# Performance work log

Measured on AMD Instinct MI355X. Metric: run time of the kernel, lower is better.

Reference implementation:

```python
import jax, jax.numpy as jnp
import numpy as np

H = 16   # num_heads
D = 16   # key_dim == output_dim (required by the module's reshape)
F = 64   # input feature dim


def setup_inputs() -> dict:
    key = jax.random.key(0)
    ks = jax.random.split(key, 8)
    B, N, Kn = 4, 4096, 32
    scale = 1.0 / np.sqrt(F)
    return {
        "inp": jax.random.normal(ks[0], (B, N, Kn, F), dtype=jnp.float32),
        "query": jax.random.normal(ks[1], (B, N, F), dtype=jnp.float32),
        "Wq": jax.random.normal(ks[2], (F, H * D), dtype=jnp.float32) * scale,
        "bq": jnp.zeros((H * D,), dtype=jnp.float32),
        "Wk": jax.random.normal(ks[3], (F, H * D), dtype=jnp.float32) * scale,
        "bk": jnp.zeros((H * D,), dtype=jnp.float32),
        "Wv": jax.random.normal(ks[4], (F, H * D), dtype=jnp.float32) * scale,
        "bv": jnp.zeros((H * D,), dtype=jnp.float32),
    }


def reference(inp, query, Wq, bq, Wk, bk, Wv, bv):
    B, N, Kn, _ = inp.shape
    # Dense projections
    Q = query @ Wq + bq                    # [B, N, H*D]
    K = inp @ Wk + bk                      # [B, N, Kn, H*D]
    V = inp @ Wv + bv                      # [B, N, Kn, H*D]
    # Faithful reshape (plain reshape of last dims, as in the TF code)
    Q = Q.reshape(B, N, H, 1, D)           # query broadcast axis of size 1
    K = K.reshape(B, N, H, Kn, D)
    V = V.reshape(B, N, H, Kn, D)
    # scaled dot-product attention per point over its Kn neighbors
    w = jnp.einsum('bnhqd,bnhkd->bnhqk', Q, K) / jnp.sqrt(jnp.float32(D))
    w = jax.nn.softmax(w, axis=-1)         # [B, N, H, 1, Kn]
    out = jnp.einsum('bnhqk,bnhkd->bnhqd', w, V)  # [B, N, H, 1, D]
    return out.reshape(B, N, H * D)
```

## Files before the change

kernel.cpp:

```cpp
#include <hip/hip_runtime.h>

#define KN 32
#define FF 64
#define CC 256
#define KV_STRIDE 260
#define VOFF (KN * KV_STRIDE)
#define NITER 16
#define QSTRIDE 264
#define WSTRIDE 36


typedef __attribute__((ext_vector_type(8)))  short bf16x8;
typedef __attribute__((ext_vector_type(16))) float f32x16;
typedef __attribute__((ext_vector_type(4)))  float f32x4;

__device__ inline unsigned short f2bf(float f) {
    union { float f; unsigned u; } v; v.f = f;
    unsigned u = v.u + 0x7fffu + ((v.u >> 16) & 1u);
    return (unsigned short)(u >> 16);
}
__device__ inline unsigned cvt_pk_bf16(float a, float b) {
    unsigned r;
    asm("v_cvt_pk_bf16_f32 %0, %1, %2" : "=v"(r) : "v"(a), "v"(b));
    return r;
}
__device__ inline bf16x8 pack8(float4 a, float4 b) {
    union { bf16x8 v; unsigned u[4]; } r;
    r.u[0] = cvt_pk_bf16(a.x, a.y);  r.u[1] = cvt_pk_bf16(a.z, a.w);
    r.u[2] = cvt_pk_bf16(b.x, b.y);  r.u[3] = cvt_pk_bf16(b.z, b.w);
    return r.v;
}

__device__ inline void lds_barrier() {
    asm volatile("s_waitcnt lgkmcnt(0)" ::: "memory");
    __builtin_amdgcn_s_barrier();
}

__global__ __launch_bounds__(256, 2)
void attn_one(const float* __restrict__ inp,
              const float* __restrict__ query,
              const float* __restrict__ Wq,
              const float* __restrict__ bq,
              const float* __restrict__ Wk,
              const float* __restrict__ bk,
              const float* __restrict__ Wv,
              const float* __restrict__ bv,
              float* __restrict__ out, int nPoints)
{
    __shared__ float kvS[2 * KN * KV_STRIDE];
    __shared__ unsigned short qAllS[NITER * QSTRIDE];
    __shared__ float wS[16 * WSTRIDE];

    const int tid  = threadIdx.x;
    const int wave = tid >> 6;
    const int L    = tid & 63;
    const int Lm   = L & 31;
    const int Lh   = L >> 5;
    const int h    = tid >> 4;
    const int d    = tid & 15;
    const int bid  = blockIdx.x;
    const int grid = gridDim.x;

    float* qIn = kvS;
    {
        const int i  = tid >> 4;
        const int f4 = (tid & 15) * 4;
        const int p  = bid + i * grid;
        if (p < nPoints)
            *(float4*)(qIn + i * 68 + f4) =
                *(const float4*)(query + (size_t)p * FF + f4);
    }

    float4 pf[8];
    {
        const float* arow = inp + (size_t)bid * (KN * FF) + Lm * FF + Lh * 8;
#pragma unroll
        for (int s = 0; s < 4; ++s) {
            pf[2 * s]     = *(const float4*)(arow + s * 16);
            pf[2 * s + 1] = *(const float4*)(arow + s * 16 + 4);
        }
    }

    bf16x8 Bf[4][4];
    float  bias[4];
#pragma unroll
    for (int t = 0; t < 4; ++t) {
        const float* W  = (t < 2) ? Wk : Wv;
        const float* bb = (t < 2) ? bk : bv;
        const int ch    = (2 * wave + (t & 1)) * 32 + Lm;
        bias[t] = bb[ch];
#pragma unroll
        for (int s = 0; s < 4; ++s) {
            union { bf16x8 v; unsigned u[4]; } r;
#pragma unroll
            for (int jj = 0; jj < 4; ++jj) {
                const int f = s * 16 + Lh * 8 + 2 * jj;
                r.u[jj] = cvt_pk_bf16(W[(size_t)f * CC + ch], W[(size_t)(f + 1) * CC + ch]);
            }
            Bf[t][s] = r.v;
        }
    }

    const int nq = L & 15;
    const int kq = (L >> 4) * 8;
    bf16x8 Bq[4][2];
    float  bqv[4];
#pragma unroll
    for (int tt = 0; tt < 4; ++tt) {
        const int ch = wave * 64 + tt * 16 + nq;
        bqv[tt] = bq[ch];
#pragma unroll
        for (int s = 0; s < 2; ++s) {
            union { bf16x8 v; unsigned u[4]; } r;
#pragma unroll
            for (int jj = 0; jj < 4; ++jj) {
                const int f = s * 32 + kq + 2 * jj;
                r.u[jj] = cvt_pk_bf16(Wq[(size_t)f * CC + ch], Wq[(size_t)(f + 1) * CC + ch]);
            }
            Bq[tt][s] = r.v;
        }
    }

    __syncthreads();

    {
        bf16x8 Aq[2];
        const int im = L & 15;
#pragma unroll
        for (int s = 0; s < 2; ++s) {
            const float* qr = qIn + im * 68 + s * 32 + kq;
            Aq[s] = pack8(*(const float4*)qr, *(const float4*)(qr + 4));
        }
#pragma unroll
        for (int tt = 0; tt < 4; ++tt) {
            f32x4 qa = {bqv[tt], bqv[tt], bqv[tt], bqv[tt]};
#pragma unroll
            for (int s = 0; s < 2; ++s)
                qa = __builtin_amdgcn_mfma_f32_16x16x32_bf16(Aq[s], Bq[tt][s], qa, 0, 0, 0);
            const int ch = wave * 64 + tt * 16 + nq;
#pragma unroll
            for (int r = 0; r < 4; ++r) {
                const int ip = (L >> 4) * 4 + r;
                qAllS[ip * QSTRIDE + ch] = f2bf(qa[r] * 0.25f);
            }
        }
    }
    __syncthreads();

    const int sR = d & 7;
    const int j0 = 2 * h + (d >> 3);

    for (int it = 0, p = bid; p < nPoints; ++it, p += grid) {
        bf16x8 Af[4];
#pragma unroll
        for (int s = 0; s < 4; ++s) Af[s] = pack8(pf[2 * s], pf[2 * s + 1]);

        const int pn = p + grid;
        if (pn < nPoints) {
            const float* arow = inp + (size_t)pn * (KN * FF) + Lm * FF + Lh * 8;
#pragma unroll
            for (int s = 0; s < 4; ++s) {
                pf[2 * s]     = *(const float4*)(arow + s * 16);
                pf[2 * s + 1] = *(const float4*)(arow + s * 16 + 4);
            }
        }

        f32x16 acc[4];
#pragma unroll
        for (int t = 0; t < 4; ++t)
#pragma unroll
            for (int r = 0; r < 16; ++r) acc[t][r] = bias[t];
#pragma unroll
        for (int s = 0; s < 4; ++s)
#pragma unroll
            for (int t = 0; t < 4; ++t)
                acc[t] = __builtin_amdgcn_mfma_f32_32x32x16_bf16(Af[s], Bf[t][s], acc[t], 0, 0, 0);

#pragma unroll
        for (int t = 0; t < 4; ++t) {
            const int s8 = 2 * wave + (t & 1);
            const int col = (t < 2)
                ? s8 * 32 + (((Lm >> 2) ^ s8) << 2) + (Lm & 3)
                : s8 * 32 + Lm;
            float* dstbase = kvS + ((t < 2) ? 0 : VOFF);
#pragma unroll
            for (int r = 0; r < 16; ++r) {
                const int jrow = (r & 3) + 8 * (r >> 2) + 4 * Lh;
                dstbase[jrow * KV_STRIDE + col] = acc[t][r];
            }
        }

        const unsigned short* qp = qAllS + it * QSTRIDE + h * 16;
        uint4 qA = *(const uint4*)qp;
        uint4 qB = *(const uint4*)(qp + 8);

        lds_barrier();

        const float* kb = kvS + j0 * KV_STRIDE + sR * 32;
        float4 ck[8];
#pragma unroll
        for (int w = 0; w < 8; ++w)
            ck[w] = *(const float4*)(kb + (((w ^ sR)) << 2));

        union { uint4 v; unsigned u[4]; } ua, ub;
        ua.v = qA;  ub.v = qB;
        float qv[16];
#pragma unroll
        for (int j = 0; j < 4; ++j) {
            qv[2 * j]     = __uint_as_float(ua.u[j] << 16);
            qv[2 * j + 1] = __uint_as_float(ua.u[j] & 0xffff0000u);
            qv[8 + 2 * j]     = __uint_as_float(ub.u[j] << 16);
            qv[8 + 2 * j + 1] = __uint_as_float(ub.u[j] & 0xffff0000u);
        }

        float l0a = 0.f, l0b = 0.f, l1a = 0.f, l1b = 0.f;
#pragma unroll
        for (int i = 0; i < 16; i += 2) {
            l0a = fmaf(qv[i],     ck[i >> 2][i & 3],             l0a);
            l0b = fmaf(qv[i + 1], ck[(i + 1) >> 2][(i + 1) & 3], l0b);
            l1a = fmaf(qv[i],     ck[4 + (i >> 2)][i & 3],             l1a);
            l1b = fmaf(qv[i + 1], ck[4 + ((i + 1) >> 2)][(i + 1) & 3], l1b);
        }
        const float l0 = l0a + l0b;
        const float l1 = l1a + l1b;

        float m = fmaxf(l0, l1);
        m = fmaxf(m, __shfl_xor(m, 1));
        m = fmaxf(m, __shfl_xor(m, 2));
        m = fmaxf(m, __shfl_xor(m, 4));
        m = fmaxf(m, __shfl_xor(m, 8));
        float e0 = __expf(l0 - m), e1 = __expf(l1 - m);
        float s2 = e0 + e1;
        s2 += __shfl_xor(s2, 1);
        s2 += __shfl_xor(s2, 2);
        s2 += __shfl_xor(s2, 4);
        s2 += __shfl_xor(s2, 8);
        const float inv = 1.0f / s2;
        *(float2*)(wS + h * WSTRIDE + 2 * d) = make_float2(e0 * inv, e1 * inv);
        __builtin_amdgcn_wave_barrier();

        float4 wv[8];
#pragma unroll
        for (int g = 0; g < 8; ++g)
            wv[g] = *(const float4*)(wS + h * WSTRIDE + 4 * g);

        const float* Vb = kvS + VOFF;
        float o0 = 0.f, o1 = 0.f, o2 = 0.f, o3 = 0.f;
#pragma unroll
        for (int k = 0; k < KN; k += 4) {
            const int jk = 2 * h + (k >> 4);
            o0 = fmaf(wv[k >> 2][0], Vb[jk * KV_STRIDE + ((k    ) & 15) * 16 + d], o0);
            o1 = fmaf(wv[k >> 2][1], Vb[jk * KV_STRIDE + ((k + 1) & 15) * 16 + d], o1);
            o2 = fmaf(wv[k >> 2][2], Vb[jk * KV_STRIDE + ((k + 2) & 15) * 16 + d], o2);
            o3 = fmaf(wv[k >> 2][3], Vb[jk * KV_STRIDE + ((k + 3) & 15) * 16 + d], o3);
        }
        out[(size_t)p * CC + tid] = (o0 + o1) + (o2 + o3);

        lds_barrier();
    }
}

extern "C" void kernel_launch(void* const* d_in, const int* in_sizes, int n_in,
                              void* d_out, int out_size, void* d_ws, size_t ws_size,
                              hipStream_t stream) {
    const float* inp   = (const float*)d_in[0];
    const float* query = (const float*)d_in[1];
    const float* Wq    = (const float*)d_in[2];
    const float* bq    = (const float*)d_in[3];
    const float* Wk    = (const float*)d_in[4];
    const float* bk    = (const float*)d_in[5];
    const float* Wv    = (const float*)d_in[6];
    const float* bv    = (const float*)d_in[7];
    float* out = (float*)d_out;

    const int nPoints = in_sizes[0] / (KN * FF);
    const int grid    = (nPoints + NITER - 1) / NITER;

    attn_one<<<grid, 256, 0, stream>>>(inp, query, Wq, bq, Wk, bk, Wv, bv,
                                       out, nPoints);
}
```

Measured before the change: 293.3 us.

## Transpose K MFMA operands and store K/V tiles to LDS with vector writes

For the K projection, the MFMA operands are swapped so the accumulator comes out transposed. Each lane can then write float4 rows into K shared memory instead of 16 scalar stores, and the XOR swizzle is dropped. V is written into a new transposed LDS layout (channel-major, stride 36) with float4 stores, and the weighted-sum loop reads V as float2 pairs. This is meant to cut LDS store instruction count and bank conflicts, but the new strides may bring different conflict patterns and the index mapping is intricate.

```diff
diff --git a/kernel.cpp b/kernel.cpp
--- a/kernel.cpp
+++ b/kernel.cpp
@@ -3,8 +3,9 @@
 #define KN 32
 #define FF 64
 #define CC 256
-#define KV_STRIDE 260
-#define VOFF (KN * KV_STRIDE)
+#define KSTR 260
+#define VST 36
+#define VTOFF (KN * KSTR)
 #define NITER 16
 #define QSTRIDE 264
 #define WSTRIDE 36
@@ -47,7 +48,7 @@
               const float* __restrict__ bv,
               float* __restrict__ out, int nPoints)
 {
-    __shared__ float kvS[2 * KN * KV_STRIDE];
+    __shared__ float kvS[KN * KSTR + CC * VST];
     __shared__ unsigned short qAllS[NITER * QSTRIDE];
     __shared__ float wS[16 * WSTRIDE];
 
@@ -82,13 +83,10 @@
     }
 
     bf16x8 Bf[4][4];
-    float  bias[4];
 #pragma unroll
     for (int t = 0; t < 4; ++t) {
         const float* W  = (t < 2) ? Wk : Wv;
-        const float* bb = (t < 2) ? bk : bv;
         const int ch    = (2 * wave + (t & 1)) * 32 + Lm;
-        bias[t] = bb[ch];
 #pragma unroll
         for (int s = 0; s < 4; ++s) {
             union { bf16x8 v; unsigned u[4]; } r;
@@ -100,6 +98,15 @@
             Bf[t][s] = r.v;
         }
     }
+    float biasV[2];
+    biasV[0] = bv[(2 * wave + 0) * 32 + Lm];
+    biasV[1] = bv[(2 * wave + 1) * 32 + Lm];
+    float4 bkK[2][4];
+#pragma unroll
+    for (int t = 0; t < 2; ++t)
+#pragma unroll
+        for (int g = 0; g < 4; ++g)
+            bkK[t][g] = *(const float4*)(bk + (2 * wave + t) * 32 + 8 * g + 4 * Lh);
 
     const int nq = L & 15;
     const int kq = (L >> 4) * 8;
@@ -167,26 +174,43 @@
 
         f32x16 acc[4];
 #pragma unroll
-        for (int t = 0; t < 4; ++t)
-#pragma unroll
-            for (int r = 0; r < 16; ++r) acc[t][r] = bias[t];
-#pragma unroll
-        for (int s = 0; s < 4; ++s)
-#pragma unroll
-            for (int t = 0; t < 4; ++t)
+        for (int t = 0; t < 2; ++t)
+#pragma unroll
+            for (int g = 0; g < 4; ++g)
+#pragma unroll
+                for (int e = 0; e < 4; ++e) acc[t][4 * g + e] = bkK[t][g][e];
+#pragma unroll
+        for (int t = 2; t < 4; ++t)
+#pragma unroll
+            for (int r = 0; r < 16; ++r) acc[t][r] = biasV[t - 2];
+
+#pragma unroll
+        for (int s = 0; s < 4; ++s) {
+#pragma unroll
+            for (int t = 0; t < 2; ++t)
+                acc[t] = __builtin_amdgcn_mfma_f32_32x32x16_bf16(Bf[t][s], Af[s], acc[t], 0, 0, 0);
+#pragma unroll
+            for (int t = 2; t < 4; ++t)
                 acc[t] = __builtin_amdgcn_mfma_f32_32x32x16_bf16(Af[s], Bf[t][s], acc[t], 0, 0, 0);
-
-#pragma unroll
-        for (int t = 0; t < 4; ++t) {
-            const int s8 = 2 * wave + (t & 1);
-            const int col = (t < 2)
-                ? s8 * 32 + (((Lm >> 2) ^ s8) << 2) + (Lm & 3)
-                : s8 * 32 + Lm;
-            float* dstbase = kvS + ((t < 2) ? 0 : VOFF);
-#pragma unroll
-            for (int r = 0; r < 16; ++r) {
-                const int jrow = (r & 3) + 8 * (r >> 2) + 4 * Lh;
-                dstbase[jrow * KV_STRIDE + col] = acc[t][r];
+        }
+
+#pragma unroll
+        for (int t = 0; t < 2; ++t) {
+            float* kr = kvS + Lm * KSTR + (2 * wave + t) * 32 + 4 * Lh;
+#pragma unroll
+            for (int g = 0; g < 4; ++g) {
+                float4 vw = {acc[t][4 * g], acc[t][4 * g + 1], acc[t][4 * g + 2], acc[t][4 * g + 3]};
+                *(float4*)(kr + 8 * g) = vw;
+            }
+        }
+#pragma unroll
+        for (int t = 2; t < 4; ++t) {
+            const int col = (2 * wave + (t & 1)) * 32 + Lm;
+            float* vr = kvS + VTOFF + col * VST + 4 * Lh;
+#pragma unroll
+            for (int g = 0; g < 4; ++g) {
+                float4 vw = {acc[t][4 * g], acc[t][4 * g + 1], acc[t][4 * g + 2], acc[t][4 * g + 3]};
+                *(float4*)(vr + 8 * g) = vw;
             }
         }
 
@@ -196,11 +220,11 @@
 
         lds_barrier();
 
-        const float* kb = kvS + j0 * KV_STRIDE + sR * 32;
+        const float* kb = kvS + j0 * KSTR + sR * 32;
         float4 ck[8];
 #pragma unroll
         for (int w = 0; w < 8; ++w)
-            ck[w] = *(const float4*)(kb + (((w ^ sR)) << 2));
+            ck[w] = *(const float4*)(kb + 4 * w);
 
         union { uint4 v; unsigned u[4]; } ua, ub;
         ua.v = qA;  ub.v = qB;
@@ -244,15 +268,16 @@
         for (int g = 0; g < 8; ++g)
             wv[g] = *(const float4*)(wS + h * WSTRIDE + 4 * g);
 
-        const float* Vb = kvS + VOFF;
+        const float* Vb = kvS + VTOFF + d * VST + 2 * h;
         float o0 = 0.f, o1 = 0.f, o2 = 0.f, o3 = 0.f;
 #pragma unroll
-        for (int k = 0; k < KN; k += 4) {
-            const int jk = 2 * h + (k >> 4);
-            o0 = fmaf(wv[k >> 2][0], Vb[jk * KV_STRIDE + ((k    ) & 15) * 16 + d], o0);
-            o1 = fmaf(wv[k >> 2][1], Vb[jk * KV_STRIDE + ((k + 1) & 15) * 16 + d], o1);
-            o2 = fmaf(wv[k >> 2][2], Vb[jk * KV_STRIDE + ((k + 2) & 15) * 16 + d], o2);
-            o3 = fmaf(wv[k >> 2][3], Vb[jk * KV_STRIDE + ((k + 3) & 15) * 16 + d], o3);
+        for (int mI = 0; mI < 16; mI += 2) {
+            const float2 va = *(const float2*)(Vb + (size_t)(16 * mI) * VST);
+            const float2 vb = *(const float2*)(Vb + (size_t)(16 * (mI + 1)) * VST);
+            o0 = fmaf(wv[mI >> 2][mI & 3],             va.x, o0);
+            o1 = fmaf(wv[4 + (mI >> 2)][mI & 3],       va.y, o1);
+            o2 = fmaf(wv[(mI + 1) >> 2][(mI + 1) & 3],       vb.x, o2);
+            o3 = fmaf(wv[4 + ((mI + 1) >> 2)][(mI + 1) & 3], vb.y, o3);
         }
         out[(size_t)p * CC + tid] = (o0 + o1) + (o2 + o3);
 
```

Measured after the change: 254.5 us. -13.2%, faster.
